# Kernel optimization log

Measured on AMD Instinct MI355X. Metric: run time of the kernel, lower is better.

## Reference

```python
import jax, jax.numpy as jnp
import numpy as np

B, S, D, H = 4, 2048, 1024, 16
HD = D // H
OUT = 256

def setup_inputs() -> dict:
    key = jax.random.key(0)
    ks = jax.random.split(key, 11)
    s = 0.02
    return {
        'query': jax.random.normal(ks[0], (B, S, D), jnp.float32),
        'key':   jax.random.normal(ks[1], (B, S, D), jnp.float32),
        'value': jax.random.normal(ks[2], (B, S, D), jnp.float32),
        'Wq': jax.random.normal(ks[3], (D, D), jnp.float32) * s,
        'bq': jnp.zeros((D,), jnp.float32),
        'Wk': jax.random.normal(ks[4], (D, D), jnp.float32) * s,
        'bk': jnp.zeros((D,), jnp.float32),
        'Wv': jax.random.normal(ks[5], (D, D), jnp.float32) * s,
        'bv': jnp.zeros((D,), jnp.float32),
        'Wf': jax.random.normal(ks[6], (D, OUT), jnp.float32) * s,
        'bf': jnp.zeros((OUT,), jnp.float32),
    }

def softmax_1(x):
    # exp(x) / (1 + sum(exp(x)))  -- numerically as written in the source
    e = jnp.exp(x)
    return e / (1.0 + e.sum(axis=-1, keepdims=True))

def reference(query, key, value, Wq, bq, Wk, bk, Wv, bv, Wf, bf):
    scale = jnp.sqrt(jnp.asarray(HD, jnp.float32))
    def heads(x, W, b):
        return (x @ W + b).reshape(B, S, H, HD).transpose(0, 2, 1, 3)  # [B,H,S,HD]
    Q = heads(query, Wq, bq)
    K = heads(key, Wk, bk)
    V = heads(value, Wv, bv)
    energy = jnp.einsum('bhqd,bhkd->bhqk', Q, K) / scale  # [B,H,S,S]
    attn = softmax_1(energy)
    x = jnp.einsum('bhqk,bhkd->bhqd', attn, V)  # dropout is identity in eval
    x = x.transpose(0, 2, 1, 3).reshape(B, S, D)
    return x @ Wf + bf  # [B,S,256]
```

## Files before the change

kernel.cpp:

```cpp
#include <hip/hip_runtime.h>
#include <stdint.h>

#define DI __device__ __forceinline__

typedef __attribute__((ext_vector_type(8))) short bf16x8;
typedef __attribute__((ext_vector_type(4))) float f32x4;
typedef __attribute__((ext_vector_type(8))) unsigned short u16x8;
typedef __attribute__((ext_vector_type(2))) unsigned int u32x2;

static constexpr int BATCH = 4, SEQ = 2048, DIM = 1024, NH = 16, HDIM = 64, DOUT = 256;
static constexpr int MROWS = BATCH * SEQ;

DI unsigned short f2b(float f) {
  union { float f; unsigned u; } v; v.f = f;
  unsigned u = v.u + 0x7FFFu + ((v.u >> 16) & 1u);
  return (unsigned short)(u >> 16);
}

DI float ex2(float x) {
#if __has_builtin(__builtin_amdgcn_exp2f)
  return __builtin_amdgcn_exp2f(x);
#else
  float r; asm("v_exp_f32 %0, %1" : "=v"(r) : "v"(x)); return r;
#endif
}

DI unsigned cvtpk(float lo, float hi) {
  unsigned r; asm("v_cvt_pk_bf16_f32 %0, %1, %2" : "=v"(r) : "v"(lo), "v"(hi)); return r;
}

typedef const __attribute__((address_space(1))) unsigned int* gp1;
typedef __attribute__((address_space(3))) unsigned int* lp3;
DI void gload16(const void* g, void* l) {
  __builtin_amdgcn_global_load_lds((gp1)g, (lp3)l, 16, 0, 0);
}

__global__ void k_cvt(const float* __restrict__ s, unsigned short* __restrict__ d, int n8) {
  int i = blockIdx.x * 256 + threadIdx.x;
  if (i >= n8) return;
  const float4* sp = reinterpret_cast<const float4*>(s) + (size_t)i * 2;
  float4 a = sp[0], b = sp[1];
  u16x8 r;
  r[0] = f2b(a.x); r[1] = f2b(a.y); r[2] = f2b(a.z); r[3] = f2b(a.w);
  r[4] = f2b(b.x); r[5] = f2b(b.y); r[6] = f2b(b.z); r[7] = f2b(b.w);
  *reinterpret_cast<u16x8*>(d + (size_t)i * 8) = r;
}

__global__ void k_tcvt(const float* __restrict__ s, unsigned short* __restrict__ d, int R, int C) {
  __shared__ float t[32][33];
  int c0 = blockIdx.x * 32, r0 = blockIdx.y * 32;
  int tx = threadIdx.x, ty = threadIdx.y;
#pragma unroll
  for (int j = 0; j < 32; j += 8)
    t[ty + j][tx] = s[(size_t)(r0 + ty + j) * C + c0 + tx];
  __syncthreads();
#pragma unroll
  for (int j = 0; j < 32; j += 8)
    d[(size_t)(c0 + ty + j) * R + r0 + tx] = f2b(t[tx][ty + j]);
}

template <int MODE>
__global__ __launch_bounds__(256, 2) void k_gemm(
    const unsigned short* __restrict__ A, const unsigned short* __restrict__ Bt,
    const float* __restrict__ bias, void* __restrict__ out, int K, int N, float scale) {
  __shared__ unsigned short Al[128 * 32];
  __shared__ unsigned short Bl[128 * 32];
  const int tid = threadIdx.x, wid = tid >> 6, lane = tid & 63;
  const int m0 = blockIdx.x * 128, n0 = blockIdx.y * 128;
  const int wr = wid >> 1, wc = wid & 1;
  const int g = lane >> 4, r16 = lane & 15;

  f32x4 acc[4][4];
#pragma unroll
  for (int i = 0; i < 4; ++i)
#pragma unroll
    for (int j = 0; j < 4; ++j) acc[i][j] = f32x4{0.f, 0.f, 0.f, 0.f};

  for (int kk = 0; kk < K; kk += 32) {
#pragma unroll
    for (int is = 0; is < 2; ++is) {
      int slot = (is * 4 + wid) * 64 + lane;
      int row = slot >> 2, ch = slot & 3;
      gload16(A + (size_t)(m0 + row) * K + kk + ch * 8, &Al[(is * 4 + wid) * 64 * 8]);
    }
#pragma unroll
    for (int is = 0; is < 2; ++is) {
      int slot = (is * 4 + wid) * 64 + lane;
      int row = slot >> 2, ch = slot & 3;
      gload16(Bt + (size_t)(n0 + row) * K + kk + ch * 8, &Bl[(is * 4 + wid) * 64 * 8]);
    }
    __syncthreads();
    bf16x8 af[4], bfv[4];
#pragma unroll
    for (int i = 0; i < 4; ++i)
      af[i] = *reinterpret_cast<const bf16x8*>(&Al[(wr * 64 + i * 16 + r16) * 32 + g * 8]);
#pragma unroll
    for (int j = 0; j < 4; ++j)
      bfv[j] = *reinterpret_cast<const bf16x8*>(&Bl[(wc * 64 + j * 16 + r16) * 32 + g * 8]);
#pragma unroll
    for (int i = 0; i < 4; ++i)
#pragma unroll
      for (int j = 0; j < 4; ++j)
        acc[i][j] = __builtin_amdgcn_mfma_f32_16x16x32_bf16(af[i], bfv[j], acc[i][j], 0, 0, 0);
    __syncthreads();
  }

  const int rr = g * 4;
#pragma unroll
  for (int i = 0; i < 4; ++i) {
#pragma unroll
    for (int j = 0; j < 4; ++j) {
#pragma unroll
      for (int q = 0; q < 4; ++q) {
        int mrow = m0 + wr * 64 + i * 16 + rr + q;
        int ncol = n0 + wc * 64 + j * 16 + r16;
        float v = (acc[i][j][q] + bias[ncol]) * scale;
        if (MODE == 0) {
          int b_ = mrow >> 11, s_ = mrow & 2047;
          int h_ = ncol >> 6, hd = ncol & 63;
          ((unsigned short*)out)[(((size_t)(b_ * NH + h_) * SEQ + s_) << 6) + hd] = f2b(v);
        } else if (MODE == 1) {
          int b_ = mrow >> 11, s_ = mrow & 2047;
          int h_ = ncol >> 6, hd = ncol & 63;
          ((unsigned short*)out)[(((size_t)(b_ * NH + h_) * HDIM + hd) << 11) + s_] = f2b(v);
        } else {
          ((float*)out)[(size_t)mrow * N + ncol] = v;
        }
      }
    }
  }
}

__global__ __launch_bounds__(256, 4) void k_attn(
    const unsigned short* __restrict__ Qh, const unsigned short* __restrict__ Kh,
    const unsigned short* __restrict__ Vt, unsigned short* __restrict__ X) {
  __shared__ unsigned short Kl[64 * 64];
  __shared__ unsigned short Vl[64 * 64];
  __shared__ unsigned short Pl[128 * 64];

  const int tid = threadIdx.x, wid = tid >> 6, lane = tid & 63;
  const int g = lane >> 4, r16 = lane & 15;
  const int bh = blockIdx.y, b_ = bh >> 4, h_ = bh & 15;
  const int q0 = blockIdx.x * 128;
  const unsigned short* Qp = Qh + ((size_t)bh * SEQ + q0) * HDIM;
  const unsigned short* Kp = Kh + (size_t)bh * SEQ * HDIM;
  const unsigned short* Vp = Vt + (size_t)bh * HDIM * SEQ;
  const int qw = wid * 32;

  bf16x8 qf[2][2];
#pragma unroll
  for (int fr = 0; fr < 2; ++fr)
#pragma unroll
    for (int ks = 0; ks < 2; ++ks)
      qf[fr][ks] = *reinterpret_cast<const bf16x8*>(
          Qp + (size_t)(qw + fr * 16 + r16) * HDIM + ks * 32 + g * 8);

  bf16x8 vones;
#pragma unroll
  for (int i = 0; i < 8; ++i) vones[i] = (r16 == 0) ? (short)0x3F80 : (short)0;

  const int slot0 = wid * 64 + lane, slot1 = (4 + wid) * 64 + lane;
  const int sr0 = slot0 >> 3, sc0 = (slot0 & 7) ^ (sr0 & 7);
  const int sr1 = slot1 >> 3, sc1 = (slot1 & 7) ^ (sr1 & 7);
  const unsigned short* Ks0 = Kp + (size_t)sr0 * HDIM + sc0 * 8;
  const unsigned short* Ks1 = Kp + (size_t)sr1 * HDIM + sc1 * 8;
  const unsigned short* Vs0 = Vp + (size_t)sr0 * SEQ + sc0 * 8;
  const unsigned short* Vs1 = Vp + (size_t)sr1 * SEQ + sc1 * 8;
  const int ld0 = wid * 512, ld1 = (4 + wid) * 512;

  f32x4 o[2][4], ol[2];
#pragma unroll
  for (int fr = 0; fr < 2; ++fr) {
#pragma unroll
    for (int hf = 0; hf < 4; ++hf) o[fr][hf] = f32x4{0.f, 0.f, 0.f, 0.f};
    ol[fr] = f32x4{0.f, 0.f, 0.f, 0.f};
  }

  for (int t = 0; t < SEQ / 64; ++t) {
    __syncthreads();
    {
      const size_t koff = (size_t)t * 64 * HDIM;
      const int voff = t * 64;
      gload16(Ks0 + koff, &Kl[ld0]);
      gload16(Ks1 + koff, &Kl[ld1]);
      gload16(Vs0 + voff, &Vl[ld0]);
      gload16(Vs1 + voff, &Vl[ld1]);
    }
    __syncthreads();

    f32x4 s_[2][4];
#pragma unroll
    for (int fr = 0; fr < 2; ++fr)
#pragma unroll
      for (int cf = 0; cf < 4; ++cf) s_[fr][cf] = f32x4{0.f, 0.f, 0.f, 0.f};
#pragma unroll
    for (int cf = 0; cf < 4; ++cf) {
      int krow = cf * 16 + r16;
#pragma unroll
      for (int ks = 0; ks < 2; ++ks) {
        bf16x8 kf = *reinterpret_cast<const bf16x8*>(
            &Kl[krow * 64 + (((ks * 4 + g) ^ (krow & 7)) << 3)]);
#pragma unroll
        for (int fr = 0; fr < 2; ++fr)
          s_[fr][cf] = __builtin_amdgcn_mfma_f32_16x16x32_bf16(kf, qf[fr][ks], s_[fr][cf], 0, 0, 0);
      }
    }

#pragma unroll
    for (int fr = 0; fr < 2; ++fr) {
      int prow = qw + fr * 16 + r16;
      int base = prow * 64, swz = prow & 7;
#pragma unroll
      for (int cf = 0; cf < 4; ++cf) {
        float p0 = ex2(s_[fr][cf][0]);
        float p1 = ex2(s_[fr][cf][1]);
        float p2 = ex2(s_[fr][cf][2]);
        float p3 = ex2(s_[fr][cf][3]);
        unsigned w0 = cvtpk(p0, p1);
        unsigned w1 = cvtpk(p2, p3);
        int off = base + (((cf * 2 + (g >> 1)) ^ swz) << 3) + (g & 1) * 4;
        *reinterpret_cast<u32x2*>(&Pl[off]) = u32x2{w0, w1};
      }
    }

#pragma unroll
    for (int ks = 0; ks < 2; ++ks) {
      bf16x8 pf[2];
#pragma unroll
      for (int fr = 0; fr < 2; ++fr) {
        int prow = qw + fr * 16 + r16;
        pf[fr] = *reinterpret_cast<const bf16x8*>(
            &Pl[prow * 64 + (((ks * 4 + g) ^ (prow & 7)) << 3)]);
      }
#pragma unroll
      for (int hf = 0; hf < 4; ++hf) {
        int vrow = hf * 16 + r16;
        bf16x8 vf = *reinterpret_cast<const bf16x8*>(
            &Vl[vrow * 64 + (((ks * 4 + g) ^ (vrow & 7)) << 3)]);
#pragma unroll
        for (int fr = 0; fr < 2; ++fr)
          o[fr][hf] = __builtin_amdgcn_mfma_f32_16x16x32_bf16(pf[fr], vf, o[fr][hf], 0, 0, 0);
      }
#pragma unroll
      for (int fr = 0; fr < 2; ++fr)
        ol[fr] = __builtin_amdgcn_mfma_f32_16x16x32_bf16(pf[fr], vones, ol[fr], 0, 0, 0);
    }
  }

#pragma unroll
  for (int fr = 0; fr < 2; ++fr) {
#pragma unroll
    for (int q = 0; q < 4; ++q) {
      float lsum = __shfl(ol[fr][q], lane & 48, 64);
      float inv = 1.0f / (1.0f + lsum);
      int row = q0 + qw + fr * 16 + g * 4 + q;
      unsigned short* xp = X + (size_t)(b_ * SEQ + row) * DIM + h_ * 64;
#pragma unroll
      for (int hf = 0; hf < 4; ++hf) xp[hf * 16 + r16] = f2b(o[fr][hf][q] * inv);
    }
  }
}

extern "C" void kernel_launch(void* const* d_in, const int* in_sizes, int n_in,
                              void* d_out, int out_size, void* d_ws, size_t ws_size,
                              hipStream_t stream) {
  const float* q  = (const float*)d_in[0];
  const float* k  = (const float*)d_in[1];
  const float* v  = (const float*)d_in[2];
  const float* Wq = (const float*)d_in[3];
  const float* bq = (const float*)d_in[4];
  const float* Wk = (const float*)d_in[5];
  const float* bk = (const float*)d_in[6];
  const float* Wv = (const float*)d_in[7];
  const float* bv = (const float*)d_in[8];
  const float* Wf = (const float*)d_in[9];
  const float* bf = (const float*)d_in[10];

  char* ws = (char*)d_ws;
  unsigned short* Abuf = (unsigned short*)ws;
  unsigned short* Wt   = (unsigned short*)(ws + (size_t)16777216);
  unsigned short* Qh   = (unsigned short*)(ws + (size_t)16777216 + 2097152);
  unsigned short* Kh   = Qh + (size_t)MROWS * DIM;
  unsigned short* Vtb  = Kh + (size_t)MROWS * DIM;

  dim3 cvtg(4096), b256(256);
  dim3 tb(32, 8);
  dim3 gemmg(64, 8);
  dim3 attng(16, 64);
  dim3 fing(64, 2);

  const int n8 = MROWS * DIM / 8;
  const float qscale = 0.125f * 1.44269504088896f;

  k_cvt<<<cvtg, b256, 0, stream>>>(q, Abuf, n8);
  k_tcvt<<<dim3(32, 32), tb, 0, stream>>>(Wq, Wt, DIM, DIM);
  k_gemm<0><<<gemmg, b256, 0, stream>>>(Abuf, Wt, bq, (void*)Qh, DIM, DIM, qscale);
  k_cvt<<<cvtg, b256, 0, stream>>>(k, Abuf, n8);
  k_tcvt<<<dim3(32, 32), tb, 0, stream>>>(Wk, Wt, DIM, DIM);
  k_gemm<0><<<gemmg, b256, 0, stream>>>(Abuf, Wt, bk, (void*)Kh, DIM, DIM, 1.0f);
  k_cvt<<<cvtg, b256, 0, stream>>>(v, Abuf, n8);
  k_tcvt<<<dim3(32, 32), tb, 0, stream>>>(Wv, Wt, DIM, DIM);
  k_gemm<1><<<gemmg, b256, 0, stream>>>(Abuf, Wt, bv, (void*)Vtb, DIM, DIM, 1.0f);
  k_attn<<<attng, b256, 0, stream>>>(Qh, Kh, Vtb, Abuf);
  k_tcvt<<<dim3(8, 32), tb, 0, stream>>>(Wf, Wt, DIM, DOUT);
  k_gemm<2><<<fing, b256, 0, stream>>>(Abuf, Wt, bf, d_out, DIM, DOUT, 1.0f);
}
```

Measured before the change: 216.8 us.

## Fuse fp32-to-bf16 activation conversion into QKV projection GEMM A-loads

```diff
diff --git a/kernel.cpp b/kernel.cpp
--- a/kernel.cpp
+++ b/kernel.cpp
@@ -7,6 +7,7 @@
 typedef __attribute__((ext_vector_type(4))) float f32x4;
 typedef __attribute__((ext_vector_type(8))) unsigned short u16x8;
 typedef __attribute__((ext_vector_type(2))) unsigned int u32x2;
+typedef __attribute__((ext_vector_type(4))) unsigned int u32x4;
 
 static constexpr int BATCH = 4, SEQ = 2048, DIM = 1024, NH = 16, HDIM = 64, DOUT = 256;
 static constexpr int MROWS = BATCH * SEQ;
@@ -35,17 +36,6 @@
   __builtin_amdgcn_global_load_lds((gp1)g, (lp3)l, 16, 0, 0);
 }
 
-__global__ void k_cvt(const float* __restrict__ s, unsigned short* __restrict__ d, int n8) {
-  int i = blockIdx.x * 256 + threadIdx.x;
-  if (i >= n8) return;
-  const float4* sp = reinterpret_cast<const float4*>(s) + (size_t)i * 2;
-  float4 a = sp[0], b = sp[1];
-  u16x8 r;
-  r[0] = f2b(a.x); r[1] = f2b(a.y); r[2] = f2b(a.z); r[3] = f2b(a.w);
-  r[4] = f2b(b.x); r[5] = f2b(b.y); r[6] = f2b(b.z); r[7] = f2b(b.w);
-  *reinterpret_cast<u16x8*>(d + (size_t)i * 8) = r;
-}
-
 __global__ void k_tcvt(const float* __restrict__ s, unsigned short* __restrict__ d, int R, int C) {
   __shared__ float t[32][33];
   int c0 = blockIdx.x * 32, r0 = blockIdx.y * 32;
@@ -59,9 +49,9 @@
     d[(size_t)(c0 + ty + j) * R + r0 + tx] = f2b(t[tx][ty + j]);
 }
 
-template <int MODE>
+template <int MODE, bool AF32>
 __global__ __launch_bounds__(256, 2) void k_gemm(
-    const unsigned short* __restrict__ A, const unsigned short* __restrict__ Bt,
+    const void* __restrict__ Ain, const unsigned short* __restrict__ Bt,
     const float* __restrict__ bias, void* __restrict__ out, int K, int N, float scale) {
   __shared__ unsigned short Al[128 * 32];
   __shared__ unsigned short Bl[128 * 32];
@@ -70,6 +60,19 @@
   const int wr = wid >> 1, wc = wid & 1;
   const int g = lane >> 4, r16 = lane & 15;
 
+  const float* Af = (const float*)Ain;
+  const unsigned short* Ab = (const unsigned short*)Ain;
+
+  const int ra = tid >> 2, ca = (tid & 3) * 8;
+  const int rb = (256 + tid) >> 2, cb = ((256 + tid) & 3) * 8;
+  float4 ar[2][2];
+  if constexpr (AF32) {
+    const float4* pa = reinterpret_cast<const float4*>(Af + (size_t)(m0 + ra) * K + ca);
+    const float4* pb = reinterpret_cast<const float4*>(Af + (size_t)(m0 + rb) * K + cb);
+    ar[0][0] = pa[0]; ar[0][1] = pa[1];
+    ar[1][0] = pb[0]; ar[1][1] = pb[1];
+  }
+
   f32x4 acc[4][4];
 #pragma unroll
   for (int i = 0; i < 4; ++i)
@@ -77,11 +80,20 @@
     for (int j = 0; j < 4; ++j) acc[i][j] = f32x4{0.f, 0.f, 0.f, 0.f};
 
   for (int kk = 0; kk < K; kk += 32) {
-#pragma unroll
-    for (int is = 0; is < 2; ++is) {
-      int slot = (is * 4 + wid) * 64 + lane;
-      int row = slot >> 2, ch = slot & 3;
-      gload16(A + (size_t)(m0 + row) * K + kk + ch * 8, &Al[(is * 4 + wid) * 64 * 8]);
+    if constexpr (AF32) {
+      u32x4 w0{cvtpk(ar[0][0].x, ar[0][0].y), cvtpk(ar[0][0].z, ar[0][0].w),
+               cvtpk(ar[0][1].x, ar[0][1].y), cvtpk(ar[0][1].z, ar[0][1].w)};
+      *reinterpret_cast<u32x4*>(&Al[ra * 32 + ca]) = w0;
+      u32x4 w1{cvtpk(ar[1][0].x, ar[1][0].y), cvtpk(ar[1][0].z, ar[1][0].w),
+               cvtpk(ar[1][1].x, ar[1][1].y), cvtpk(ar[1][1].z, ar[1][1].w)};
+      *reinterpret_cast<u32x4*>(&Al[rb * 32 + cb]) = w1;
+    } else {
+#pragma unroll
+      for (int is = 0; is < 2; ++is) {
+        int slot = (is * 4 + wid) * 64 + lane;
+        int row = slot >> 2, ch = slot & 3;
+        gload16(Ab + (size_t)(m0 + row) * K + kk + ch * 8, &Al[(is * 4 + wid) * 64 * 8]);
+      }
     }
 #pragma unroll
     for (int is = 0; is < 2; ++is) {
@@ -90,6 +102,14 @@
       gload16(Bt + (size_t)(n0 + row) * K + kk + ch * 8, &Bl[(is * 4 + wid) * 64 * 8]);
     }
     __syncthreads();
+    if constexpr (AF32) {
+      if (kk + 32 < K) {
+        const float4* pa = reinterpret_cast<const float4*>(Af + (size_t)(m0 + ra) * K + kk + 32 + ca);
+        const float4* pb = reinterpret_cast<const float4*>(Af + (size_t)(m0 + rb) * K + kk + 32 + cb);
+        ar[0][0] = pa[0]; ar[0][1] = pa[1];
+        ar[1][0] = pb[0]; ar[1][1] = pb[1];
+      }
+    }
     bf16x8 af[4], bfv[4];
 #pragma unroll
     for (int i = 0; i < 4; ++i)
@@ -283,25 +303,21 @@
   unsigned short* Kh   = Qh + (size_t)MROWS * DIM;
   unsigned short* Vtb  = Kh + (size_t)MROWS * DIM;
 
-  dim3 cvtg(4096), b256(256);
+  dim3 b256(256);
   dim3 tb(32, 8);
   dim3 gemmg(64, 8);
   dim3 attng(16, 64);
   dim3 fing(64, 2);
 
-  const int n8 = MROWS * DIM / 8;
   const float qscale = 0.125f * 1.44269504088896f;
 
-  k_cvt<<<cvtg, b256, 0, stream>>>(q, Abuf, n8);
   k_tcvt<<<dim3(32, 32), tb, 0, stream>>>(Wq, Wt, DIM, DIM);
-  k_gemm<0><<<gemmg, b256, 0, stream>>>(Abuf, Wt, bq, (void*)Qh, DIM, DIM, qscale);
-  k_cvt<<<cvtg, b256, 0, stream>>>(k, Abuf, n8);
+  k_gemm<0, true><<<gemmg, b256, 0, stream>>>(q, Wt, bq, (void*)Qh, DIM, DIM, qscale);
   k_tcvt<<<dim3(32, 32), tb, 0, stream>>>(Wk, Wt, DIM, DIM);
-  k_gemm<0><<<gemmg, b256, 0, stream>>>(Abuf, Wt, bk, (void*)Kh, DIM, DIM, 1.0f);
-  k_cvt<<<cvtg, b256, 0, stream>>>(v, Abuf, n8);
+  k_gemm<0, true><<<gemmg, b256, 0, stream>>>(k, Wt, bk, (void*)Kh, DIM, DIM, 1.0f);
   k_tcvt<<<dim3(32, 32), tb, 0, stream>>>(Wv, Wt, DIM, DIM);
-  k_gemm<1><<<gemmg, b256, 0, stream>>>(Abuf, Wt, bv, (void*)Vtb, DIM, DIM, 1.0f);
+  k_gemm<1, true><<<gemmg, b256, 0, stream>>>(v, Wt, bv, (void*)Vtb, DIM, DIM, 1.0f);
   k_attn<<<attng, b256, 0, stream>>>(Qh, Kh, Vtb, Abuf);
   k_tcvt<<<dim3(8, 32), tb, 0, stream>>>(Wf, Wt, DIM, DOUT);
-  k_gemm<2><<<fing, b256, 0, stream>>>(Abuf, Wt, bf, d_out, DIM, DOUT, 1.0f);
-}
+  k_gemm<2, false><<<fing, b256, 0, stream>>>(Abuf, Wt, bf, d_out, DIM, DOUT, 1.0f);
+}
```

After: 204.0 us. 5.9% less time.
